# Optimization experiments

Hardware: AMD Instinct MI355X
Metric: run time of the kernel (lower is better)

Reference implementation:

```python
import jax, jax.numpy as jnp
import numpy as np

N_NODES = 50000


def sage_conv(x, src, dst, Wl, bl, Wr):
    # PyG SAGEConv (aggr='mean'): out = lin_l(mean_{j in N(i)} x_j) + lin_r(x_i)
    # lin_l has bias, lin_r (root) has no bias.
    n = x.shape[0]
    agg = jax.ops.segment_sum(x[src], dst, num_segments=n)          # [N, d_in]
    cnt = jax.ops.segment_sum(jnp.ones((src.shape[0],), x.dtype), dst, num_segments=n)
    mean = agg / jnp.maximum(cnt, 1.0)[:, None]
    return mean @ Wl + bl + x @ Wr


def setup_inputs() -> dict:
    key = jax.random.key(0)
    k1, k2, k3, k4, k5, k6, k7 = jax.random.split(key, 7)
    in_c, hid_c, out_c = 128, 128, 2
    x = jax.random.normal(k1, (N_NODES, in_c), dtype=jnp.float32)
    edge_index = jax.random.randint(k2, (2, 800000), 0, N_NODES, dtype=jnp.int64)
    s1 = 1.0 / np.sqrt(in_c)
    s2 = 1.0 / np.sqrt(hid_c)
    return {
        "x": x,
        "edge_index": edge_index,
        "W1l": jax.random.uniform(k3, (in_c, hid_c), jnp.float32, -s1, s1),
        "b1l": jnp.zeros((hid_c,), jnp.float32),
        "W1r": jax.random.uniform(k4, (in_c, hid_c), jnp.float32, -s1, s1),
        "W2l": jax.random.uniform(k5, (hid_c, out_c), jnp.float32, -s2, s2),
        "b2l": jnp.zeros((out_c,), jnp.float32),
        "W2r": jax.random.uniform(k6, (hid_c, out_c), jnp.float32, -s2, s2),
    }


def reference(x, edge_index, W1l, b1l, W1r, W2l, b2l, W2r):
    src, dst = edge_index[0], edge_index[1]
    h = jax.nn.relu(sage_conv(x, src, dst, W1l, b1l, W1r))
    return sage_conv(h, src, dst, W2l, b2l, W2r)
```

## Files before the change

kernel.cpp:

```cpp
#include <hip/hip_runtime.h>

#define N_NODES 50000
#define N_PAD 50176
#define N_EDGES 800000
#define C 128
#define NB 784
#define NPB 64
#define CBCAP 1408
#define B1_BUCK 391
#define TOBF_B 6250
#define ZPAD_B 11
#define PACK_B 16
#define PLANE_U ((size_t)N_PAD * 32)
#define GS_B 6272

typedef unsigned short ushort_t;
typedef unsigned int uint_t;
typedef __attribute__((ext_vector_type(8))) short bf16x8;
typedef __attribute__((ext_vector_type(4))) float f32x4;

__device__ __forceinline__ uint_t f2bf(float f) {
    uint_t u = __float_as_uint(f);
    u += 0x7fffu + ((u >> 16) & 1u);
    return u >> 16;
}
__device__ __forceinline__ float bflo(uint_t u) { return __uint_as_float(u << 16); }
__device__ __forceinline__ float bfhi(uint_t u) { return __uint_as_float(u & 0xffff0000u); }

__global__ __launch_bounds__(256) void bucket1_kernel(
    const int* __restrict__ src, const int* __restrict__ dst,
    int* __restrict__ gcur, uint_t* __restrict__ cb,
    const float* __restrict__ x, ushort_t* __restrict__ xh,
    const float* __restrict__ W1l, const float* __restrict__ W1r,
    ushort_t* __restrict__ Bp) {
    int b = blockIdx.x;
    int t = threadIdx.x;
    if (b < B1_BUCK) {
        __shared__ int hist[NB];
        __shared__ int offs[NB];
        for (int i = t; i < NB; i += 256) hist[i] = 0;
        __syncthreads();
        int tid = b * 256 + t;
        bool act = tid < N_EDGES / 8;
        int4 s0, s1, d0, d1;
        if (act) {
            s0 = ((const int4*)src)[2 * tid];
            s1 = ((const int4*)src)[2 * tid + 1];
            d0 = ((const int4*)dst)[2 * tid];
            d1 = ((const int4*)dst)[2 * tid + 1];
            atomicAdd(&hist[d0.x >> 6], 1);
            atomicAdd(&hist[d0.y >> 6], 1);
            atomicAdd(&hist[d0.z >> 6], 1);
            atomicAdd(&hist[d0.w >> 6], 1);
            atomicAdd(&hist[d1.x >> 6], 1);
            atomicAdd(&hist[d1.y >> 6], 1);
            atomicAdd(&hist[d1.z >> 6], 1);
            atomicAdd(&hist[d1.w >> 6], 1);
        }
        __syncthreads();
        for (int i = t; i < NB; i += 256) {
            offs[i] = atomicAdd(&gcur[i], hist[i]);
            hist[i] = 0;
        }
        __syncthreads();
        if (act) {
            int ss[8] = {s0.x, s0.y, s0.z, s0.w, s1.x, s1.y, s1.z, s1.w};
            int dd[8] = {d0.x, d0.y, d0.z, d0.w, d1.x, d1.y, d1.z, d1.w};
            #pragma unroll
            for (int i = 0; i < 8; i++) {
                int bkt = dd[i] >> 6;
                int pos = offs[bkt] + atomicAdd(&hist[bkt], 1);
                if (pos < CBCAP)
                    cb[(size_t)bkt * CBCAP + pos] = ((uint_t)ss[i] << 16) | (uint_t)dd[i];
            }
        }
    } else if (b < B1_BUCK + TOBF_B) {
        int i = (b - B1_BUCK) * 256 + t;
        float4 v = ((const float4*)x)[i];
        uint_t lo = f2bf(v.x) | (f2bf(v.y) << 16);
        uint_t hi = f2bf(v.z) | (f2bf(v.w) << 16);
        int node = i >> 5, c = i & 31;
        int plane = c >> 3, part = c & 7;
        ((uint2*)(xh + (size_t)plane * PLANE_U + node * 32 + part * 4))[0] =
            make_uint2(lo, hi);
    } else if (b < B1_BUCK + TOBF_B + ZPAD_B) {
        int i = (b - B1_BUCK - TOBF_B) * 256 + t;
        if (i < 2816) {
            int plane = i / 704, rem = i % 704;
            int node = N_NODES + (rem >> 2), part = rem & 3;
            ((uint4*)(xh + (size_t)plane * PLANE_U + node * 32 + part * 8))[0] =
                make_uint4(0, 0, 0, 0);
        }
    } else {
        int p = (b - B1_BUCK - TOBF_B - ZPAD_B) * 256 + t;
        int lane = p & 63;
        int pair = p >> 6;
        int kk = pair & 7;
        int nt = pair >> 3;
        int n = lane & 15, quad = lane >> 4;
        int col = nt * 16 + n;
        int k0 = kk * 32 + quad * 8;
        uint_t w[4];
        #pragma unroll
        for (int jj = 0; jj < 4; jj++) {
            int ka = k0 + 2 * jj, kb = k0 + 2 * jj + 1;
            float fa = (ka < C) ? W1l[ka * C + col] : W1r[(ka - C) * C + col];
            float fb = (kb < C) ? W1l[kb * C + col] : W1r[(kb - C) * C + col];
            w[jj] = f2bf(fa) | (f2bf(fb) << 16);
        }
        ((uint4*)(Bp + (size_t)p * 8))[0] = make_uint4(w[0], w[1], w[2], w[3]);
    }
}

__global__ __launch_bounds__(256) void sort_kernel(
    const int* __restrict__ gcur, const uint_t* __restrict__ cb,
    ushort_t* __restrict__ esorted, int* __restrict__ nodeoff,
    int* __restrict__ cursor) {
    __shared__ uint_t srun[CBCAP];
    __shared__ ushort_t sidx[CBCAP];
    __shared__ int cnt[NPB], offs[NPB], cur[NPB];
    int b = blockIdx.x, t = threadIdx.x;
    if (t < NPB) { cnt[t] = 0; cur[t] = 0; }
    __syncthreads();

    int len = gcur[b];
    if (len > CBCAP) len = CBCAP;
    const uint_t* run = cb + (size_t)b * CBCAP;
    for (int e = t; e < len; e += 256) {
        uint_t rec = run[e];
        srun[e] = rec;
        atomicAdd(&cnt[rec & (NPB - 1)], 1);
    }
    __syncthreads();

    if (t < 64) {
        int v = cnt[t];
        int s = v;
        #pragma unroll
        for (int o = 1; o < 64; o <<= 1) {
            int u = __shfl_up(s, o, 64);
            if (t >= o) s += u;
        }
        offs[t] = s - v;
    }
    __syncthreads();

    for (int e = t; e < len; e += 256) {
        uint_t rec = srun[e];
        int local = rec & (NPB - 1);
        int pos = offs[local] + atomicAdd(&cur[local], 1);
        sidx[pos] = (ushort_t)(rec >> 16);
    }
    __syncthreads();

    for (int e = t; 2 * e < len; e += 256) {
        uint_t v = (uint_t)sidx[2 * e];
        if (2 * e + 1 < len) v |= (uint_t)sidx[2 * e + 1] << 16;
        ((uint_t*)esorted)[(size_t)b * (CBCAP / 2) + e] = v;
    }
    if (t < NPB) {
        int g = b * NPB + t;
        nodeoff[g] = b * CBCAP + offs[t];
        cursor[g] = cnt[t];
    }
}

__device__ __forceinline__ void bf8_acc(float* a, const uint4 v) {
    a[0] += bflo(v.x); a[1] += bfhi(v.x);
    a[2] += bflo(v.y); a[3] += bfhi(v.y);
    a[4] += bflo(v.z); a[5] += bfhi(v.z);
    a[6] += bflo(v.w); a[7] += bfhi(v.w);
}

__global__ __launch_bounds__(128) void gather_slice(
    const ushort_t* __restrict__ xh, const ushort_t* __restrict__ esorted,
    const int* __restrict__ nodeoff, const int* __restrict__ cursor,
    ushort_t* __restrict__ msb) {
    int b = blockIdx.x, t = threadIdx.x;
    int slice = (b & 7) >> 1;
    int chunk = (b >> 3) * 2 + (b & 1);
    int g = t >> 2, lane = t & 3;
    int node = chunk * 32 + g;
    int d = cursor[node];
    const ushort_t* lst = esorted + nodeoff[node];
    const ushort_t* plane = xh + (size_t)slice * PLANE_U + lane * 8;

    float a[8] = {0,0,0,0,0,0,0,0};
    float c8[8] = {0,0,0,0,0,0,0,0};
    int e = 0;
    for (; e + 8 <= d; e += 8) {
        int s0 = lst[e + 0], s1 = lst[e + 1], s2 = lst[e + 2], s3 = lst[e + 3];
        int s4 = lst[e + 4], s5 = lst[e + 5], s6 = lst[e + 6], s7 = lst[e + 7];
        uint4 v0 = *(const uint4*)(plane + (size_t)s0 * 32);
        uint4 v1 = *(const uint4*)(plane + (size_t)s1 * 32);
        uint4 v2 = *(const uint4*)(plane + (size_t)s2 * 32);
        uint4 v3 = *(const uint4*)(plane + (size_t)s3 * 32);
        uint4 v4 = *(const uint4*)(plane + (size_t)s4 * 32);
        uint4 v5 = *(const uint4*)(plane + (size_t)s5 * 32);
        uint4 v6 = *(const uint4*)(plane + (size_t)s6 * 32);
        uint4 v7 = *(const uint4*)(plane + (size_t)s7 * 32);
        bf8_acc(a, v0); bf8_acc(c8, v1); bf8_acc(a, v2); bf8_acc(c8, v3);
        bf8_acc(a, v4); bf8_acc(c8, v5); bf8_acc(a, v6); bf8_acc(c8, v7);
    }
    for (; e + 4 <= d; e += 4) {
        int s0 = lst[e + 0], s1 = lst[e + 1], s2 = lst[e + 2], s3 = lst[e + 3];
        uint4 v0 = *(const uint4*)(plane + (size_t)s0 * 32);
        uint4 v1 = *(const uint4*)(plane + (size_t)s1 * 32);
        uint4 v2 = *(const uint4*)(plane + (size_t)s2 * 32);
        uint4 v3 = *(const uint4*)(plane + (size_t)s3 * 32);
        bf8_acc(a, v0); bf8_acc(c8, v1); bf8_acc(a, v2); bf8_acc(c8, v3);
    }
    for (; e < d; e++) {
        uint4 v = *(const uint4*)(plane + (size_t)lst[e] * 32);
        bf8_acc(a, v);
    }
    float inv = 1.0f / fmaxf((float)d, 1.0f);
    uint4 o;
    o.x = f2bf((a[0] + c8[0]) * inv) | (f2bf((a[1] + c8[1]) * inv) << 16);
    o.y = f2bf((a[2] + c8[2]) * inv) | (f2bf((a[3] + c8[3]) * inv) << 16);
    o.z = f2bf((a[4] + c8[4]) * inv) | (f2bf((a[5] + c8[5]) * inv) << 16);
    o.w = f2bf((a[6] + c8[6]) * inv) | (f2bf((a[7] + c8[7]) * inv) << 16);
    ((uint4*)(msb + (size_t)node * C + slice * 32 + lane * 8))[0] = o;
}

__global__ __launch_bounds__(512) void gemm_mfma(
    const ushort_t* __restrict__ msb, const ushort_t* __restrict__ xh,
    const ushort_t* __restrict__ Bp, const float* __restrict__ b1l,
    const float* __restrict__ W2l, const float* __restrict__ W2r,
    const float* __restrict__ b2l, float* __restrict__ z, float* __restrict__ out) {
    __shared__ ushort_t sB[2 * C * C];
    int t = threadIdx.x;
    #pragma unroll
    for (int i = 0; i < 8; i++)
        ((uint4*)sB)[i * 512 + t] = ((const uint4*)Bp)[i * 512 + t];
    __syncthreads();

    int wid = t >> 6, lane = t & 63;
    int m = lane & 15, quad = lane >> 4;
    int base = blockIdx.x * 128 + wid * 16;
    int node = base + m;

    const ushort_t* a_ms = msb + (size_t)node * C + quad * 8;
    bf16x8 aw[8];
    #pragma unroll
    for (int kk = 0; kk < 4; kk++) aw[kk] = *(const bf16x8*)(a_ms + kk * 32);
    #pragma unroll
    for (int kk = 0; kk < 4; kk++)
        aw[4 + kk] = *(const bf16x8*)(xh + (size_t)kk * PLANE_U + node * 32 + quad * 8);

    f32x4 acc[8];
    #pragma unroll
    for (int nt = 0; nt < 8; nt++) acc[nt] = (f32x4){0.f, 0.f, 0.f, 0.f};

    const bf16x8* bp = (const bf16x8*)sB;
    #pragma unroll
    for (int kk = 0; kk < 8; kk++) {
        bf16x8 a = aw[kk];
        #pragma unroll
        for (int nt = 0; nt < 8; nt++) {
            bf16x8 bfr = bp[(nt * 8 + kk) * 64 + lane];
            acc[nt] = __builtin_amdgcn_mfma_f32_16x16x32_bf16(a, bfr, acc[nt], 0, 0, 0);
        }
    }

    float zz0[4] = {0,0,0,0}, zz1[4] = {0,0,0,0};
    float rr0[4] = {0,0,0,0}, rr1[4] = {0,0,0,0};
    #pragma unroll
    for (int nt = 0; nt < 8; nt++) {
        int col = nt * 16 + m;
        float bias = b1l[col];
        float2 wl = ((const float2*)W2l)[col];
        float2 wr = ((const float2*)W2r)[col];
        #pragma unroll
        for (int reg = 0; reg < 4; reg++) {
            float h = fmaxf(acc[nt][reg] + bias, 0.0f);
            zz0[reg] = fmaf(h, wl.x, zz0[reg]);
            zz1[reg] = fmaf(h, wl.y, zz1[reg]);
            rr0[reg] = fmaf(h, wr.x, rr0[reg]);
            rr1[reg] = fmaf(h, wr.y, rr1[reg]);
        }
    }
    float bl0 = b2l[0], bl1 = b2l[1];
    #pragma unroll
    for (int reg = 0; reg < 4; reg++) {
        float a0 = zz0[reg], a1 = zz1[reg], c0 = rr0[reg], c1 = rr1[reg];
        #pragma unroll
        for (int off = 8; off > 0; off >>= 1) {
            a0 += __shfl_down(a0, off, 16);
            a1 += __shfl_down(a1, off, 16);
            c0 += __shfl_down(c0, off, 16);
            c1 += __shfl_down(c1, off, 16);
        }
        if (m == 0) {
            int onode = base + quad * 4 + reg;
            if (onode < N_NODES) {
                z[onode * 2 + 0]   = a0;
                z[onode * 2 + 1]   = a1;
                out[onode * 2 + 0] = c0 + bl0;
                out[onode * 2 + 1] = c1 + bl1;
            }
        }
    }
}

__global__ __launch_bounds__(256) void final_kernel(
    const float* __restrict__ z, const int* __restrict__ nodeoff,
    const int* __restrict__ cursor, const ushort_t* __restrict__ esorted,
    float* __restrict__ out) {
    int t = threadIdx.x;
    int sub = t & 15;
    int node = blockIdx.x * 16 + (t >> 4);
    int d = cursor[node];
    const ushort_t* lst = esorted + nodeoff[node];
    float a0 = 0.0f, a1 = 0.0f;
    for (int e = sub; e < d; e += 16) {
        float2 v = ((const float2*)z)[lst[e]];
        a0 += v.x; a1 += v.y;
    }
    #pragma unroll
    for (int off = 8; off > 0; off >>= 1) {
        a0 += __shfl_down(a0, off);
        a1 += __shfl_down(a1, off);
    }
    if (sub == 0) {
        float inv = 1.0f / fmaxf((float)d, 1.0f);
        out[node * 2 + 0] += a0 * inv;
        out[node * 2 + 1] += a1 * inv;
    }
}

extern "C" void kernel_launch(void* const* d_in, const int* in_sizes, int n_in,
                              void* d_out, int out_size, void* d_ws, size_t ws_size,
                              hipStream_t stream) {
    const float* x   = (const float*)d_in[0];
    const int*   ei  = (const int*)d_in[1];
    const float* W1l = (const float*)d_in[2];
    const float* b1l = (const float*)d_in[3];
    const float* W1r = (const float*)d_in[4];
    const float* W2l = (const float*)d_in[5];
    const float* b2l = (const float*)d_in[6];
    const float* W2r = (const float*)d_in[7];
    float* out = (float*)d_out;

    const int* src = ei;
    const int* dst = ei + N_EDGES;

    int* gcur         = (int*)d_ws;
    uint_t* cb        = (uint_t*)(gcur + 1024);
    ushort_t* esorted = (ushort_t*)(cb + (size_t)NB * CBCAP);
    int* nodeoff      = (int*)(esorted + (size_t)NB * CBCAP);
    int* cursor       = nodeoff + N_PAD;
    ushort_t* xh      = (ushort_t*)(cursor + N_PAD);
    ushort_t* msb     = xh + 4 * PLANE_U;
    ushort_t* Bp      = msb + (size_t)N_PAD * C;
    float* z          = (float*)(Bp + 2 * C * C);

    hipMemsetAsync(gcur, 0, NB * sizeof(int), stream);

    bucket1_kernel<<<B1_BUCK + TOBF_B + ZPAD_B + PACK_B, 256, 0, stream>>>(
        src, dst, gcur, cb, x, xh, W1l, W1r, Bp);
    sort_kernel<<<NB, 256, 0, stream>>>(gcur, cb, esorted, nodeoff, cursor);
    gather_slice<<<GS_B, 128, 0, stream>>>(xh, esorted, nodeoff, cursor, msb);
    gemm_mfma<<<392, 512, 0, stream>>>(msb, xh, Bp, b1l, W2l, W2r, b2l, z, out);
    final_kernel<<<N_NODES / 16, 256, 0, stream>>>(z, nodeoff, cursor, esorted, out);
}
```

Before: 149.9 us.

## Replace bucket-sort CSR build with per-node atomic slotting into padded lists

Drops the two-stage bucket histogram and sort kernel and instead builds per-node neighbor lists directly. Each edge does a global atomicAdd on its destination's cursor and writes its source into a fixed 48-slot padded row. The gather and final kernels read these padded rows. This removes a kernel launch and the intermediate bucket buffer round-trip, but adds many scattered global atomics and silently truncates nodes whose degree exceeds 48.

```diff
diff --git a/kernel.cpp b/kernel.cpp
--- a/kernel.cpp
+++ b/kernel.cpp
@@ -4,10 +4,8 @@
 #define N_PAD 50176
 #define N_EDGES 800000
 #define C 128
-#define NB 784
-#define NPB 64
-#define CBCAP 1408
-#define B1_BUCK 391
+#define CAP 48
+#define SC_B 782
 #define TOBF_B 6250
 #define ZPAD_B 11
 #define PACK_B 16
@@ -27,55 +25,29 @@
 __device__ __forceinline__ float bflo(uint_t u) { return __uint_as_float(u << 16); }
 __device__ __forceinline__ float bfhi(uint_t u) { return __uint_as_float(u & 0xffff0000u); }
 
-__global__ __launch_bounds__(256) void bucket1_kernel(
+__global__ __launch_bounds__(256) void prep_kernel(
     const int* __restrict__ src, const int* __restrict__ dst,
-    int* __restrict__ gcur, uint_t* __restrict__ cb,
+    int* __restrict__ cursor, ushort_t* __restrict__ epad,
     const float* __restrict__ x, ushort_t* __restrict__ xh,
     const float* __restrict__ W1l, const float* __restrict__ W1r,
     ushort_t* __restrict__ Bp) {
     int b = blockIdx.x;
     int t = threadIdx.x;
-    if (b < B1_BUCK) {
-        __shared__ int hist[NB];
-        __shared__ int offs[NB];
-        for (int i = t; i < NB; i += 256) hist[i] = 0;
-        __syncthreads();
+    if (b < SC_B) {
         int tid = b * 256 + t;
-        bool act = tid < N_EDGES / 8;
-        int4 s0, s1, d0, d1;
-        if (act) {
-            s0 = ((const int4*)src)[2 * tid];
-            s1 = ((const int4*)src)[2 * tid + 1];
-            d0 = ((const int4*)dst)[2 * tid];
-            d1 = ((const int4*)dst)[2 * tid + 1];
-            atomicAdd(&hist[d0.x >> 6], 1);
-            atomicAdd(&hist[d0.y >> 6], 1);
-            atomicAdd(&hist[d0.z >> 6], 1);
-            atomicAdd(&hist[d0.w >> 6], 1);
-            atomicAdd(&hist[d1.x >> 6], 1);
-            atomicAdd(&hist[d1.y >> 6], 1);
-            atomicAdd(&hist[d1.z >> 6], 1);
-            atomicAdd(&hist[d1.w >> 6], 1);
-        }
-        __syncthreads();
-        for (int i = t; i < NB; i += 256) {
-            offs[i] = atomicAdd(&gcur[i], hist[i]);
-            hist[i] = 0;
-        }
-        __syncthreads();
-        if (act) {
-            int ss[8] = {s0.x, s0.y, s0.z, s0.w, s1.x, s1.y, s1.z, s1.w};
-            int dd[8] = {d0.x, d0.y, d0.z, d0.w, d1.x, d1.y, d1.z, d1.w};
+        if (tid < N_EDGES / 4) {
+            int4 s4 = ((const int4*)src)[tid];
+            int4 d4 = ((const int4*)dst)[tid];
+            int ss[4] = {s4.x, s4.y, s4.z, s4.w};
+            int dd[4] = {d4.x, d4.y, d4.z, d4.w};
             #pragma unroll
-            for (int i = 0; i < 8; i++) {
-                int bkt = dd[i] >> 6;
-                int pos = offs[bkt] + atomicAdd(&hist[bkt], 1);
-                if (pos < CBCAP)
-                    cb[(size_t)bkt * CBCAP + pos] = ((uint_t)ss[i] << 16) | (uint_t)dd[i];
+            for (int i = 0; i < 4; i++) {
+                int pos = atomicAdd(&cursor[dd[i]], 1);
+                if (pos < CAP) epad[dd[i] * CAP + pos] = (ushort_t)ss[i];
             }
         }
-    } else if (b < B1_BUCK + TOBF_B) {
-        int i = (b - B1_BUCK) * 256 + t;
+    } else if (b < SC_B + TOBF_B) {
+        int i = (b - SC_B) * 256 + t;
         float4 v = ((const float4*)x)[i];
         uint_t lo = f2bf(v.x) | (f2bf(v.y) << 16);
         uint_t hi = f2bf(v.z) | (f2bf(v.w) << 16);
@@ -83,8 +55,8 @@
         int plane = c >> 3, part = c & 7;
         ((uint2*)(xh + (size_t)plane * PLANE_U + node * 32 + part * 4))[0] =
             make_uint2(lo, hi);
-    } else if (b < B1_BUCK + TOBF_B + ZPAD_B) {
-        int i = (b - B1_BUCK - TOBF_B) * 256 + t;
+    } else if (b < SC_B + TOBF_B + ZPAD_B) {
+        int i = (b - SC_B - TOBF_B) * 256 + t;
         if (i < 2816) {
             int plane = i / 704, rem = i % 704;
             int node = N_NODES + (rem >> 2), part = rem & 3;
@@ -92,7 +64,7 @@
                 make_uint4(0, 0, 0, 0);
         }
     } else {
-        int p = (b - B1_BUCK - TOBF_B - ZPAD_B) * 256 + t;
+        int p = (b - SC_B - TOBF_B - ZPAD_B) * 256 + t;
         int lane = p & 63;
         int pair = p >> 6;
         int kk = pair & 7;
@@ -112,59 +84,6 @@
     }
 }
 
-__global__ __launch_bounds__(256) void sort_kernel(
-    const int* __restrict__ gcur, const uint_t* __restrict__ cb,
-    ushort_t* __restrict__ esorted, int* __restrict__ nodeoff,
-    int* __restrict__ cursor) {
-    __shared__ uint_t srun[CBCAP];
-    __shared__ ushort_t sidx[CBCAP];
-    __shared__ int cnt[NPB], offs[NPB], cur[NPB];
-    int b = blockIdx.x, t = threadIdx.x;
-    if (t < NPB) { cnt[t] = 0; cur[t] = 0; }
-    __syncthreads();
-
-    int len = gcur[b];
-    if (len > CBCAP) len = CBCAP;
-    const uint_t* run = cb + (size_t)b * CBCAP;
-    for (int e = t; e < len; e += 256) {
-        uint_t rec = run[e];
-        srun[e] = rec;
-        atomicAdd(&cnt[rec & (NPB - 1)], 1);
-    }
-    __syncthreads();
-
-    if (t < 64) {
-        int v = cnt[t];
-        int s = v;
-        #pragma unroll
-        for (int o = 1; o < 64; o <<= 1) {
-            int u = __shfl_up(s, o, 64);
-            if (t >= o) s += u;
-        }
-        offs[t] = s - v;
-    }
-    __syncthreads();
-
-    for (int e = t; e < len; e += 256) {
-        uint_t rec = srun[e];
-        int local = rec & (NPB - 1);
-        int pos = offs[local] + atomicAdd(&cur[local], 1);
-        sidx[pos] = (ushort_t)(rec >> 16);
-    }
-    __syncthreads();
-
-    for (int e = t; 2 * e < len; e += 256) {
-        uint_t v = (uint_t)sidx[2 * e];
-        if (2 * e + 1 < len) v |= (uint_t)sidx[2 * e + 1] << 16;
-        ((uint_t*)esorted)[(size_t)b * (CBCAP / 2) + e] = v;
-    }
-    if (t < NPB) {
-        int g = b * NPB + t;
-        nodeoff[g] = b * CBCAP + offs[t];
-        cursor[g] = cnt[t];
-    }
-}
-
 __device__ __forceinline__ void bf8_acc(float* a, const uint4 v) {
     a[0] += bflo(v.x); a[1] += bfhi(v.x);
     a[2] += bflo(v.y); a[3] += bfhi(v.y);
@@ -173,22 +92,22 @@
 }
 
 __global__ __launch_bounds__(128) void gather_slice(
-    const ushort_t* __restrict__ xh, const ushort_t* __restrict__ esorted,
-    const int* __restrict__ nodeoff, const int* __restrict__ cursor,
-    ushort_t* __restrict__ msb) {
+    const ushort_t* __restrict__ xh, const ushort_t* __restrict__ epad,
+    const int* __restrict__ cursor, ushort_t* __restrict__ msb) {
     int b = blockIdx.x, t = threadIdx.x;
     int slice = (b & 7) >> 1;
     int chunk = (b >> 3) * 2 + (b & 1);
     int g = t >> 2, lane = t & 3;
     int node = chunk * 32 + g;
     int d = cursor[node];
-    const ushort_t* lst = esorted + nodeoff[node];
+    int dd = d < CAP ? d : CAP;
+    const ushort_t* lst = epad + node * CAP;
     const ushort_t* plane = xh + (size_t)slice * PLANE_U + lane * 8;
 
     float a[8] = {0,0,0,0,0,0,0,0};
     float c8[8] = {0,0,0,0,0,0,0,0};
     int e = 0;
-    for (; e + 8 <= d; e += 8) {
+    for (; e + 8 <= dd; e += 8) {
         int s0 = lst[e + 0], s1 = lst[e + 1], s2 = lst[e + 2], s3 = lst[e + 3];
         int s4 = lst[e + 4], s5 = lst[e + 5], s6 = lst[e + 6], s7 = lst[e + 7];
         uint4 v0 = *(const uint4*)(plane + (size_t)s0 * 32);
@@ -202,7 +121,7 @@
         bf8_acc(a, v0); bf8_acc(c8, v1); bf8_acc(a, v2); bf8_acc(c8, v3);
         bf8_acc(a, v4); bf8_acc(c8, v5); bf8_acc(a, v6); bf8_acc(c8, v7);
     }
-    for (; e + 4 <= d; e += 4) {
+    for (; e + 4 <= dd; e += 4) {
         int s0 = lst[e + 0], s1 = lst[e + 1], s2 = lst[e + 2], s3 = lst[e + 3];
         uint4 v0 = *(const uint4*)(plane + (size_t)s0 * 32);
         uint4 v1 = *(const uint4*)(plane + (size_t)s1 * 32);
@@ -210,7 +129,7 @@
         uint4 v3 = *(const uint4*)(plane + (size_t)s3 * 32);
         bf8_acc(a, v0); bf8_acc(c8, v1); bf8_acc(a, v2); bf8_acc(c8, v3);
     }
-    for (; e < d; e++) {
+    for (; e < dd; e++) {
         uint4 v = *(const uint4*)(plane + (size_t)lst[e] * 32);
         bf8_acc(a, v);
     }
@@ -304,16 +223,16 @@
 }
 
 __global__ __launch_bounds__(256) void final_kernel(
-    const float* __restrict__ z, const int* __restrict__ nodeoff,
-    const int* __restrict__ cursor, const ushort_t* __restrict__ esorted,
-    float* __restrict__ out) {
+    const float* __restrict__ z, const ushort_t* __restrict__ epad,
+    const int* __restrict__ cursor, float* __restrict__ out) {
     int t = threadIdx.x;
     int sub = t & 15;
     int node = blockIdx.x * 16 + (t >> 4);
     int d = cursor[node];
-    const ushort_t* lst = esorted + nodeoff[node];
+    int dd = d < CAP ? d : CAP;
+    const ushort_t* lst = epad + node * CAP;
     float a0 = 0.0f, a1 = 0.0f;
-    for (int e = sub; e < d; e += 16) {
+    for (int e = sub; e < dd; e += 16) {
         float2 v = ((const float2*)z)[lst[e]];
         a0 += v.x; a1 += v.y;
     }
@@ -345,22 +264,18 @@
     const int* src = ei;
     const int* dst = ei + N_EDGES;
 
-    int* gcur         = (int*)d_ws;
-    uint_t* cb        = (uint_t*)(gcur + 1024);
-    ushort_t* esorted = (ushort_t*)(cb + (size_t)NB * CBCAP);
-    int* nodeoff      = (int*)(esorted + (size_t)NB * CBCAP);
-    int* cursor       = nodeoff + N_PAD;
-    ushort_t* xh      = (ushort_t*)(cursor + N_PAD);
-    ushort_t* msb     = xh + 4 * PLANE_U;
-    ushort_t* Bp      = msb + (size_t)N_PAD * C;
-    float* z          = (float*)(Bp + 2 * C * C);
-
-    hipMemsetAsync(gcur, 0, NB * sizeof(int), stream);
-
-    bucket1_kernel<<<B1_BUCK + TOBF_B + ZPAD_B + PACK_B, 256, 0, stream>>>(
-        src, dst, gcur, cb, x, xh, W1l, W1r, Bp);
-    sort_kernel<<<NB, 256, 0, stream>>>(gcur, cb, esorted, nodeoff, cursor);
-    gather_slice<<<GS_B, 128, 0, stream>>>(xh, esorted, nodeoff, cursor, msb);
+    int* cursor    = (int*)d_ws;
+    ushort_t* epad = (ushort_t*)(cursor + N_PAD);
+    ushort_t* xh   = epad + (size_t)N_PAD * CAP;
+    ushort_t* msb  = xh + 4 * PLANE_U;
+    ushort_t* Bp   = msb + (size_t)N_PAD * C;
+    float* z       = (float*)(Bp + 2 * C * C);
+
+    hipMemsetAsync(cursor, 0, N_PAD * sizeof(int), stream);
+
+    prep_kernel<<<SC_B + TOBF_B + ZPAD_B + PACK_B, 256, 0, stream>>>(
+        src, dst, cursor, epad, x, xh, W1l, W1r, Bp);
+    gather_slice<<<GS_B, 128, 0, stream>>>(xh, epad, cursor, msb);
     gemm_mfma<<<392, 512, 0, stream>>>(msb, xh, Bp, b1l, W2l, W2r, b2l, z, out);
-    final_kernel<<<N_NODES / 16, 256, 0, stream>>>(z, nodeoff, cursor, esorted, out);
-}
+    final_kernel<<<N_NODES / 16, 256, 0, stream>>>(z, epad, cursor, out);
+}
```

Measured after the change: 184.3 us. 1.23x slower.
